# Kernel tuning notes

Hardware: AMD Instinct MI355X
Metric: run time of the kernel (lower is better)

Reference implementation:

```python
import jax, jax.numpy as jnp
import numpy as np

N = 50000
E = 600000
LLM_DIM = 640
HIDDEN = 128
STRUCT_DIM = 16
N_STRUCT_TYPES = 5
N_LAYERS = 2
LN_EPS = 1e-5


def setup_inputs() -> dict:
    key = jax.random.key(0)
    ks = jax.random.split(key, 10)
    llm_feat = jax.random.normal(ks[0], (N, LLM_DIM), dtype=jnp.float32)
    struct_type_ids = jax.random.randint(ks[1], (N,), 0, N_STRUCT_TYPES, dtype=jnp.int64)
    edge_index = jax.random.randint(ks[2], (2, E), 0, N, dtype=jnp.int64)
    proj_out = HIDDEN - STRUCT_DIM  # 112
    proj_W = jax.random.normal(ks[3], (LLM_DIM, proj_out), dtype=jnp.float32) / np.sqrt(LLM_DIM)
    proj_b = jnp.zeros((proj_out,), dtype=jnp.float32)
    struct_emb = jax.random.normal(ks[4], (N_STRUCT_TYPES, STRUCT_DIM), dtype=jnp.float32)
    gcn_W = jax.random.normal(ks[5], (N_LAYERS, HIDDEN, HIDDEN), dtype=jnp.float32) / np.sqrt(HIDDEN)
    gcn_b = jnp.zeros((N_LAYERS, HIDDEN), dtype=jnp.float32)
    ln_g = jnp.ones((HIDDEN,), dtype=jnp.float32)
    ln_b = jnp.zeros((HIDDEN,), dtype=jnp.float32)
    return dict(llm_feat=llm_feat, struct_type_ids=struct_type_ids, edge_index=edge_index,
                proj_W=proj_W, proj_b=proj_b, struct_emb=struct_emb,
                gcn_W=gcn_W, gcn_b=gcn_b, ln_g=ln_g, ln_b=ln_b)


def _gcn_conv(x, src, dst, deg_inv_sqrt, W, b):
    """PyG GCNConv: x' = D^{-1/2}(A+I)D^{-1/2} (x W) + b, D over A+I."""
    xw = x @ W  # [N, H]
    norm = deg_inv_sqrt[src] * deg_inv_sqrt[dst]  # [E]
    msg = xw[src] * norm[:, None]  # [E, H]
    agg = jax.ops.segment_sum(msg, dst, num_segments=N)  # [N, H]
    # self-loop contribution: norm_ii = deg_i^{-1}
    agg = agg + xw * (deg_inv_sqrt * deg_inv_sqrt)[:, None]
    return agg + b


def reference(llm_feat, struct_type_ids, edge_index, proj_W, proj_b,
              struct_emb, gcn_W, gcn_b, ln_g, ln_b):
    x_llm = llm_feat @ proj_W + proj_b  # [N, hidden-struct_dim]
    x_struct = struct_emb[struct_type_ids]  # [N, struct_dim]
    x = jnp.concatenate([x_llm, x_struct], axis=-1)  # [N, hidden]

    src, dst = edge_index[0], edge_index[1]
    # degree with self-loops (A + I)
    deg = 1.0 + jax.ops.segment_sum(jnp.ones((E,), dtype=x.dtype), dst, num_segments=N)
    deg_inv_sqrt = jax.lax.rsqrt(deg)

    for l in range(N_LAYERS):
        x_new = jax.nn.relu(_gcn_conv(x, src, dst, deg_inv_sqrt, gcn_W[l], gcn_b[l]))
        # dropout is identity in eval mode
        x = x + x_new

    mean = jnp.mean(x, axis=-1, keepdims=True)
    var = jnp.mean(jnp.square(x - mean), axis=-1, keepdims=True)
    return (x - mean) * jax.lax.rsqrt(var + LN_EPS) * ln_g + ln_b
```

## Files before the change

kernel.cpp:

```cpp
#include <hip/hip_runtime.h>

#define N_NODES 50000
#define E_EDGES 600000
#define LLM_DIM 640
#define HIDDEN 128
#define POUT 112
#define NB_SCAN 98

typedef __attribute__((ext_vector_type(8))) short bf16x8;
typedef __attribute__((ext_vector_type(4))) float f32x4;

__device__ inline unsigned short f2bf(float f) {
    unsigned u = __float_as_uint(f);
    u += 0x7fff + ((u >> 16) & 1);
    return (unsigned short)(u >> 16);
}
__device__ inline float bflo(unsigned v) { return __uint_as_float(v << 16); }
__device__ inline float bfhi(unsigned v) { return __uint_as_float(v & 0xffff0000u); }

__global__ void deg_count(const int* __restrict__ eidx, int* __restrict__ cnt) {
    int e = blockIdx.x * 256 + threadIdx.x;
    if (e < E_EDGES) atomicAdd(&cnt[eidx[E_EDGES + e]], 1);
}

__global__ void make_dis(const int* __restrict__ cnt, float* __restrict__ dis) {
    int i = blockIdx.x * 256 + threadIdx.x;
    if (i < N_NODES) dis[i] = rsqrtf(1.0f + (float)cnt[i]);
}

__global__ __launch_bounds__(256) void scan_blocksum(const int* __restrict__ cnt, int* __restrict__ bsum) {
    __shared__ int s[256];
    int b = blockIdx.x, t = threadIdx.x;
    int i0 = b * 512 + t, i1 = i0 + 256;
    int v = (i0 < N_NODES ? cnt[i0] : 0) + (i1 < N_NODES ? cnt[i1] : 0);
    s[t] = v;
    __syncthreads();
    for (int st = 128; st; st >>= 1) {
        if (t < st) s[t] += s[t + st];
        __syncthreads();
    }
    if (t == 0) bsum[b] = s[0];
}

__global__ void scan_bsum(const int* __restrict__ bsum, int* __restrict__ bpre) {
    __shared__ int s[128];
    int t = threadIdx.x;
    if (t < NB_SCAN) s[t] = bsum[t];
    __syncthreads();
    if (t == 0) {
        int a = 0;
        for (int i = 0; i < NB_SCAN; i++) { int v = s[i]; s[i] = a; a += v; }
    }
    __syncthreads();
    if (t < NB_SCAN) bpre[t] = s[t];
}

__global__ __launch_bounds__(256) void scan_offs(const int* __restrict__ cnt, const int* __restrict__ bpre,
                                                 int* __restrict__ offs) {
    __shared__ int sA[512], sB[512];
    int b = blockIdx.x, t = threadIdx.x;
    int i0 = b * 512 + t, i1 = i0 + 256;
    int v0 = (i0 < N_NODES ? cnt[i0] : 0);
    int v1 = (i1 < N_NODES ? cnt[i1] : 0);
    sA[t] = v0; sA[t + 256] = v1;
    int* src = sA; int* dst = sB;
    for (int st = 1; st < 512; st <<= 1) {
        __syncthreads();
        dst[t]       = src[t]       + (t       >= st ? src[t - st]       : 0);
        dst[t + 256] = src[t + 256] + (t + 256 >= st ? src[t + 256 - st] : 0);
        int* tmp = src; src = dst; dst = tmp;
    }
    __syncthreads();
    int base = bpre[b];
    if (i0 < N_NODES) offs[i0] = base + src[t] - v0;
    if (i1 < N_NODES) offs[i1] = base + src[t + 256] - v1;
    if (b == 0 && t == 0) offs[N_NODES] = E_EDGES;
}

__global__ void fill_srcs(const int* __restrict__ eidx, const int* __restrict__ offs,
                          int* __restrict__ pos, int* __restrict__ srcs) {
    int e = blockIdx.x * 256 + threadIdx.x;
    if (e >= E_EDGES) return;
    int s = eidx[e];
    int d = eidx[E_EDGES + e];
    int p = atomicAdd(&pos[d], 1);
    srcs[offs[d] + p] = s;
}

__global__ void wt_convert(const float* __restrict__ W, unsigned short* __restrict__ Wt) {
    int idx = blockIdx.x * 256 + threadIdx.x;
    if (idx >= POUT * LLM_DIM) return;
    int n = idx / LLM_DIM;
    int k = idx - n * LLM_DIM;
    Wt[(size_t)n * LLM_DIM + k] = f2bf(W[(size_t)k * POUT + n]);
}

__global__ void w2_convert(const float* __restrict__ W, unsigned short* __restrict__ Wt2) {
    int idx = blockIdx.x * 256 + threadIdx.x;
    if (idx >= 2 * HIDDEN * HIDDEN) return;
    int l = idx >> 14;
    int rem = idx & 16383;
    int n = rem >> 7;
    int k = rem & 127;
    Wt2[idx] = f2bf(W[l * 16384 + k * 128 + n]);
}

__global__ __launch_bounds__(256) void proj_mfma(const float* __restrict__ A,
                                                 const unsigned short* __restrict__ Wt,
                                                 const float* __restrict__ bias,
                                                 const float* __restrict__ emb,
                                                 const int* __restrict__ sid,
                                                 const float* __restrict__ dis,
                                                 float* __restrict__ X,
                                                 unsigned short* __restrict__ Xs) {
    __shared__ short As[64][72];
    __shared__ short Bs[112][72];
    const int tid = threadIdx.x;
    const int wave = tid >> 6, lane = tid & 63;
    const int row0 = blockIdx.x * 64;
    const int l15 = lane & 15, l4 = lane >> 4;

    f32x4 acc[7];
#pragma unroll
    for (int j = 0; j < 7; j++) acc[j] = (f32x4){0.f, 0.f, 0.f, 0.f};

    for (int k0 = 0; k0 < LLM_DIM; k0 += 64) {
#pragma unroll
        for (int i = 0; i < 4; i++) {
            int f = i * 256 + tid;
            int r = f >> 4;
            int q = f & 15;
            int grow = row0 + r;
            float4 v = make_float4(0.f, 0.f, 0.f, 0.f);
            if (grow < N_NODES)
                v = *reinterpret_cast<const float4*>(A + (size_t)grow * LLM_DIM + k0 + q * 4);
            uint2 u;
            u.x = (unsigned)f2bf(v.x) | ((unsigned)f2bf(v.y) << 16);
            u.y = (unsigned)f2bf(v.z) | ((unsigned)f2bf(v.w) << 16);
            *reinterpret_cast<uint2*>(&As[r][q * 4]) = u;
        }
#pragma unroll
        for (int i = 0; i < 7; i++) {
            int f = i * 256 + tid;
            int n = f >> 4;
            int q = f & 15;
            uint2 v = *reinterpret_cast<const uint2*>(Wt + (size_t)n * LLM_DIM + k0 + q * 4);
            *reinterpret_cast<uint2*>(&Bs[n][q * 4]) = v;
        }
        __syncthreads();
#pragma unroll
        for (int ks = 0; ks < 2; ks++) {
            int kk = ks * 32 + l4 * 8;
            bf16x8 a = *reinterpret_cast<bf16x8*>(&As[wave * 16 + l15][kk]);
#pragma unroll
            for (int ct = 0; ct < 7; ct++) {
                bf16x8 b = *reinterpret_cast<bf16x8*>(&Bs[ct * 16 + l15][kk]);
                acc[ct] = __builtin_amdgcn_mfma_f32_16x16x32_bf16(a, b, acc[ct], 0, 0, 0);
            }
        }
        __syncthreads();
    }
#pragma unroll
    for (int r = 0; r < 4; r++) {
        int row = row0 + wave * 16 + l4 * 4 + r;
        if (row >= N_NODES) continue;
        float d = dis[row];
#pragma unroll
        for (int ct = 0; ct < 7; ct++) {
            int col = ct * 16 + l15;
            float v = acc[ct][r] + bias[col];
            X[(size_t)row * HIDDEN + col] = v;
            Xs[(size_t)row * HIDDEN + col] = f2bf(d * v);
        }
        float e = emb[sid[row] * 16 + l15];
        X[(size_t)row * HIDDEN + POUT + l15] = e;
        Xs[(size_t)row * HIDDEN + POUT + l15] = f2bf(d * e);
    }
}

__global__ __launch_bounds__(256) void gather(const unsigned short* __restrict__ Xs,
                                              const int* __restrict__ offs,
                                              const int* __restrict__ srcs,
                                              const float* __restrict__ dis,
                                              unsigned short* __restrict__ Gb) {
    int node = blockIdx.x * 4 + (threadIdx.x >> 6);
    int lane = threadIdx.x & 63;
    if (node >= N_NODES) return;
    int beg = __builtin_amdgcn_readfirstlane(offs[node]);
    int end = __builtin_amdgcn_readfirstlane(offs[node + 1]);
    const unsigned* X32 = reinterpret_cast<const unsigned*>(Xs);
    float ax = 0.f, ay = 0.f;
    int e = beg;
    while (e < end) {
        int n = end - e;
        if (n > 64) n = 64;
        int idx = (lane < n) ? srcs[e + lane] : 0;
        int j = 0;
        for (; j + 4 <= n; j += 4) {
            int s0 = __shfl(idx, j);
            int s1 = __shfl(idx, j + 1);
            int s2 = __shfl(idx, j + 2);
            int s3 = __shfl(idx, j + 3);
            unsigned v0 = X32[(size_t)s0 * 64 + lane];
            unsigned v1 = X32[(size_t)s1 * 64 + lane];
            unsigned v2 = X32[(size_t)s2 * 64 + lane];
            unsigned v3 = X32[(size_t)s3 * 64 + lane];
            ax += (bflo(v0) + bflo(v1)) + (bflo(v2) + bflo(v3));
            ay += (bfhi(v0) + bfhi(v1)) + (bfhi(v2) + bfhi(v3));
        }
        for (; j < n; j++) {
            int s = __shfl(idx, j);
            unsigned v = X32[(size_t)s * 64 + lane];
            ax += bflo(v);
            ay += bfhi(v);
        }
        e += 64;
    }
    float d = dis[node];
    unsigned sv = X32[(size_t)node * 64 + lane];
    ax = d * (ax + bflo(sv));
    ay = d * (ay + bfhi(sv));
    reinterpret_cast<unsigned*>(Gb)[(size_t)node * 64 + lane] =
        (unsigned)f2bf(ax) | ((unsigned)f2bf(ay) << 16);
}

template <int MODE>
__global__ __launch_bounds__(256) void gemm_fin(const unsigned short* __restrict__ Gb,
                                                const unsigned short* __restrict__ Wt2,
                                                const float* __restrict__ bias,
                                                const float* __restrict__ dis,
                                                const float* __restrict__ lng,
                                                const float* __restrict__ lnb,
                                                float* __restrict__ X,
                                                unsigned short* __restrict__ Xs2) {
    __shared__ short As[64][136];
    __shared__ short Bs[128][136];
    const int tid = threadIdx.x;
    const int wave = tid >> 6, lane = tid & 63;
    const int row0 = blockIdx.x * 64;
    const int l15 = lane & 15, l4 = lane >> 4;

#pragma unroll
    for (int i = 0; i < 4; i++) {
        int f = i * 256 + tid;
        int r = f >> 4;
        int q = f & 15;
        int grow = row0 + r;
        uint4 v = make_uint4(0, 0, 0, 0);
        if (grow < N_NODES)
            v = reinterpret_cast<const uint4*>(Gb + (size_t)grow * HIDDEN)[q];
        *reinterpret_cast<uint4*>(&As[r][q * 8]) = v;
    }
#pragma unroll
    for (int i = 0; i < 8; i++) {
        int f = i * 256 + tid;
        int r = f >> 4;
        int q = f & 15;
        uint4 v = reinterpret_cast<const uint4*>(Wt2 + (size_t)r * HIDDEN)[q];
        *reinterpret_cast<uint4*>(&Bs[r][q * 8]) = v;
    }
    __syncthreads();

    f32x4 acc[8];
#pragma unroll
    for (int j = 0; j < 8; j++) acc[j] = (f32x4){0.f, 0.f, 0.f, 0.f};
#pragma unroll
    for (int ks = 0; ks < 4; ks++) {
        int kk = ks * 32 + l4 * 8;
        bf16x8 a = *reinterpret_cast<bf16x8*>(&As[wave * 16 + l15][kk]);
#pragma unroll
        for (int ct = 0; ct < 8; ct++) {
            bf16x8 b = *reinterpret_cast<bf16x8*>(&Bs[ct * 16 + l15][kk]);
            acc[ct] = __builtin_amdgcn_mfma_f32_16x16x32_bf16(a, b, acc[ct], 0, 0, 0);
        }
    }

    float bcol[8];
#pragma unroll
    for (int ct = 0; ct < 8; ct++) bcol[ct] = bias[ct * 16 + l15];

    float vv[8][4];
#pragma unroll
    for (int r = 0; r < 4; r++) {
        int row = row0 + wave * 16 + l4 * 4 + r;
        bool ok = row < N_NODES;
#pragma unroll
        for (int ct = 0; ct < 8; ct++) {
            float xo = ok ? X[(size_t)row * HIDDEN + ct * 16 + l15] : 0.f;
            vv[ct][r] = xo + fmaxf(acc[ct][r] + bcol[ct], 0.f);
        }
    }

    if (MODE == 0) {
#pragma unroll
        for (int r = 0; r < 4; r++) {
            int row = row0 + wave * 16 + l4 * 4 + r;
            if (row >= N_NODES) continue;
            float d = dis[row];
#pragma unroll
            for (int ct = 0; ct < 8; ct++) {
                int col = ct * 16 + l15;
                X[(size_t)row * HIDDEN + col] = vv[ct][r];
                Xs2[(size_t)row * HIDDEN + col] = f2bf(d * vv[ct][r]);
            }
        }
    } else {
        float s[4], q2[4];
#pragma unroll
        for (int r = 0; r < 4; r++) {
            s[r] = 0.f; q2[r] = 0.f;
#pragma unroll
            for (int ct = 0; ct < 8; ct++) {
                s[r] += vv[ct][r];
                q2[r] += vv[ct][r] * vv[ct][r];
            }
        }
#pragma unroll
        for (int off = 1; off < 16; off <<= 1) {
#pragma unroll
            for (int r = 0; r < 4; r++) {
                s[r] += __shfl_xor(s[r], off);
                q2[r] += __shfl_xor(q2[r], off);
            }
        }
        float gcol[8], bcol2[8];
#pragma unroll
        for (int ct = 0; ct < 8; ct++) {
            gcol[ct] = lng[ct * 16 + l15];
            bcol2[ct] = lnb[ct * 16 + l15];
        }
#pragma unroll
        for (int r = 0; r < 4; r++) {
            int row = row0 + wave * 16 + l4 * 4 + r;
            if (row >= N_NODES) continue;
            float mean = s[r] * (1.f / 128.f);
            float var = q2[r] * (1.f / 128.f) - mean * mean;
            float inv = rsqrtf(var + 1e-5f);
#pragma unroll
            for (int ct = 0; ct < 8; ct++) {
                int col = ct * 16 + l15;
                X[(size_t)row * HIDDEN + col] = (vv[ct][r] - mean) * inv * gcol[ct] + bcol2[ct];
            }
        }
    }
}

extern "C" void kernel_launch(void* const* d_in, const int* in_sizes, int n_in,
                              void* d_out, int out_size, void* d_ws, size_t ws_size,
                              hipStream_t stream) {
    const float* llm   = (const float*)d_in[0];
    const int*   sid   = (const int*)d_in[1];
    const int*   eidx  = (const int*)d_in[2];
    const float* projW = (const float*)d_in[3];
    const float* projb = (const float*)d_in[4];
    const float* emb   = (const float*)d_in[5];
    const float* gcnW  = (const float*)d_in[6];
    const float* gcnb  = (const float*)d_in[7];
    const float* lng   = (const float*)d_in[8];
    const float* lnb   = (const float*)d_in[9];

    float* X = (float*)d_out;
    unsigned short* Xs = (unsigned short*)d_ws;
    unsigned short* Gb = Xs + (size_t)N_NODES * HIDDEN;
    unsigned short* Wt = Gb;
    unsigned short* Wt2 = Gb + (size_t)N_NODES * HIDDEN;
    float* dis = (float*)(Wt2 + 2 * HIDDEN * HIDDEN);
    int* cnt  = (int*)(dis + N_NODES);
    int* offs = cnt + N_NODES;
    int* bsum = offs + N_NODES + 1;
    int* bpre = bsum + 128;
    int* srcs = bpre + 128;

    hipMemsetAsync(cnt, 0, N_NODES * sizeof(int), stream);
    deg_count<<<(E_EDGES + 255) / 256, 256, 0, stream>>>(eidx, cnt);
    make_dis<<<(N_NODES + 255) / 256, 256, 0, stream>>>(cnt, dis);
    scan_blocksum<<<NB_SCAN, 256, 0, stream>>>(cnt, bsum);
    scan_bsum<<<1, 128, 0, stream>>>(bsum, bpre);
    scan_offs<<<NB_SCAN, 256, 0, stream>>>(cnt, bpre, offs);
    hipMemsetAsync(cnt, 0, N_NODES * sizeof(int), stream);
    fill_srcs<<<(E_EDGES + 255) / 256, 256, 0, stream>>>(eidx, offs, cnt, srcs);

    wt_convert<<<(POUT * LLM_DIM + 255) / 256, 256, 0, stream>>>(projW, Wt);
    w2_convert<<<(2 * HIDDEN * HIDDEN + 255) / 256, 256, 0, stream>>>(gcnW, Wt2);

    proj_mfma<<<(N_NODES + 63) / 64, 256, 0, stream>>>(llm, Wt, projb, emb, sid, dis, X, Xs);

    gather<<<(N_NODES + 3) / 4, 256, 0, stream>>>(Xs, offs, srcs, dis, Gb);
    gemm_fin<0><<<(N_NODES + 63) / 64, 256, 0, stream>>>(Gb, Wt2, gcnb, dis, lng, lnb, X, Xs);
    gather<<<(N_NODES + 3) / 4, 256, 0, stream>>>(Xs, offs, srcs, dis, Gb);
    gemm_fin<1><<<(N_NODES + 63) / 64, 256, 0, stream>>>(Gb, Wt2 + HIDDEN * HIDDEN, gcnb + HIDDEN, dis, lng, lnb, X, Xs);
}
```

Baseline: 389.5 us.

## Merge weight conversions, fold memsets, unroll gather deeper, prefetch residual in GEMM

```diff
diff --git a/kernel.cpp b/kernel.cpp
--- a/kernel.cpp
+++ b/kernel.cpp
@@ -87,22 +87,23 @@
     srcs[offs[d] + p] = s;
 }
 
-__global__ void wt_convert(const float* __restrict__ W, unsigned short* __restrict__ Wt) {
+__global__ void conv_weights(const float* __restrict__ Wp, const float* __restrict__ Wg,
+                             unsigned short* __restrict__ Wt, unsigned short* __restrict__ Wt2) {
     int idx = blockIdx.x * 256 + threadIdx.x;
-    if (idx >= POUT * LLM_DIM) return;
-    int n = idx / LLM_DIM;
-    int k = idx - n * LLM_DIM;
-    Wt[(size_t)n * LLM_DIM + k] = f2bf(W[(size_t)k * POUT + n]);
-}
-
-__global__ void w2_convert(const float* __restrict__ W, unsigned short* __restrict__ Wt2) {
-    int idx = blockIdx.x * 256 + threadIdx.x;
-    if (idx >= 2 * HIDDEN * HIDDEN) return;
-    int l = idx >> 14;
-    int rem = idx & 16383;
-    int n = rem >> 7;
-    int k = rem & 127;
-    Wt2[idx] = f2bf(W[l * 16384 + k * 128 + n]);
+    if (idx < POUT * LLM_DIM) {
+        int n = idx / LLM_DIM;
+        int k = idx - n * LLM_DIM;
+        Wt[(size_t)n * LLM_DIM + k] = f2bf(Wp[(size_t)k * POUT + n]);
+    } else {
+        int i2 = idx - POUT * LLM_DIM;
+        if (i2 < 2 * HIDDEN * HIDDEN) {
+            int l = i2 >> 14;
+            int rem = i2 & 16383;
+            int n = rem >> 7;
+            int k = rem & 127;
+            Wt2[i2] = f2bf(Wg[l * 16384 + k * 128 + n]);
+        }
+    }
 }
 
 __global__ __launch_bounds__(256) void proj_mfma(const float* __restrict__ A,
@@ -189,6 +190,8 @@
     int beg = __builtin_amdgcn_readfirstlane(offs[node]);
     int end = __builtin_amdgcn_readfirstlane(offs[node + 1]);
     const unsigned* X32 = reinterpret_cast<const unsigned*>(Xs);
+    float d = dis[node];
+    unsigned sv = X32[(size_t)node * 64 + lane];
     float ax = 0.f, ay = 0.f;
     int e = beg;
     while (e < end) {
@@ -196,7 +199,29 @@
         if (n > 64) n = 64;
         int idx = (lane < n) ? srcs[e + lane] : 0;
         int j = 0;
-        for (; j + 4 <= n; j += 4) {
+        for (; j + 8 <= n; j += 8) {
+            int s0 = __shfl(idx, j);
+            int s1 = __shfl(idx, j + 1);
+            int s2 = __shfl(idx, j + 2);
+            int s3 = __shfl(idx, j + 3);
+            int s4 = __shfl(idx, j + 4);
+            int s5 = __shfl(idx, j + 5);
+            int s6 = __shfl(idx, j + 6);
+            int s7 = __shfl(idx, j + 7);
+            unsigned v0 = X32[(size_t)s0 * 64 + lane];
+            unsigned v1 = X32[(size_t)s1 * 64 + lane];
+            unsigned v2 = X32[(size_t)s2 * 64 + lane];
+            unsigned v3 = X32[(size_t)s3 * 64 + lane];
+            unsigned v4 = X32[(size_t)s4 * 64 + lane];
+            unsigned v5 = X32[(size_t)s5 * 64 + lane];
+            unsigned v6 = X32[(size_t)s6 * 64 + lane];
+            unsigned v7 = X32[(size_t)s7 * 64 + lane];
+            ax += ((bflo(v0) + bflo(v1)) + (bflo(v2) + bflo(v3)))
+                + ((bflo(v4) + bflo(v5)) + (bflo(v6) + bflo(v7)));
+            ay += ((bfhi(v0) + bfhi(v1)) + (bfhi(v2) + bfhi(v3)))
+                + ((bfhi(v4) + bfhi(v5)) + (bfhi(v6) + bfhi(v7)));
+        }
+        if (j + 4 <= n) {
             int s0 = __shfl(idx, j);
             int s1 = __shfl(idx, j + 1);
             int s2 = __shfl(idx, j + 2);
@@ -207,17 +232,21 @@
             unsigned v3 = X32[(size_t)s3 * 64 + lane];
             ax += (bflo(v0) + bflo(v1)) + (bflo(v2) + bflo(v3));
             ay += (bfhi(v0) + bfhi(v1)) + (bfhi(v2) + bfhi(v3));
-        }
-        for (; j < n; j++) {
-            int s = __shfl(idx, j);
-            unsigned v = X32[(size_t)s * 64 + lane];
-            ax += bflo(v);
-            ay += bfhi(v);
+            j += 4;
+        }
+        int rem = n - j;
+        if (rem > 0) {
+            int s0 = __shfl(idx, j);
+            int s1 = __shfl(idx, j + (rem > 1 ? 1 : 0));
+            int s2 = __shfl(idx, j + (rem > 2 ? 2 : 0));
+            unsigned v0 = X32[(size_t)s0 * 64 + lane];
+            unsigned v1 = X32[(size_t)s1 * 64 + lane];
+            unsigned v2 = X32[(size_t)s2 * 64 + lane];
+            ax += bflo(v0) + (rem > 1 ? bflo(v1) : 0.f) + (rem > 2 ? bflo(v2) : 0.f);
+            ay += bfhi(v0) + (rem > 1 ? bfhi(v1) : 0.f) + (rem > 2 ? bfhi(v2) : 0.f);
         }
         e += 64;
     }
-    float d = dis[node];
-    unsigned sv = X32[(size_t)node * 64 + lane];
     ax = d * (ax + bflo(sv));
     ay = d * (ay + bfhi(sv));
     reinterpret_cast<unsigned*>(Gb)[(size_t)node * 64 + lane] =
@@ -259,6 +288,17 @@
         uint4 v = reinterpret_cast<const uint4*>(Wt2 + (size_t)r * HIDDEN)[q];
         *reinterpret_cast<uint4*>(&Bs[r][q * 8]) = v;
     }
+
+    float xo[8][4];
+#pragma unroll
+    for (int r = 0; r < 4; r++) {
+        int row = row0 + wave * 16 + l4 * 4 + r;
+        int rc = row < N_NODES ? row : 0;
+#pragma unroll
+        for (int ct = 0; ct < 8; ct++)
+            xo[ct][r] = X[(size_t)rc * HIDDEN + ct * 16 + l15];
+    }
+
     __syncthreads();
 
     f32x4 acc[8];
@@ -286,8 +326,8 @@
         bool ok = row < N_NODES;
 #pragma unroll
         for (int ct = 0; ct < 8; ct++) {
-            float xo = ok ? X[(size_t)row * HIDDEN + ct * 16 + l15] : 0.f;
-            vv[ct][r] = xo + fmaxf(acc[ct][r] + bcol[ct], 0.f);
+            float xv = ok ? xo[ct][r] : 0.f;
+            vv[ct][r] = xv + fmaxf(acc[ct][r] + bcol[ct], 0.f);
         }
     }
 
@@ -366,22 +406,21 @@
     unsigned short* Wt2 = Gb + (size_t)N_NODES * HIDDEN;
     float* dis = (float*)(Wt2 + 2 * HIDDEN * HIDDEN);
     int* cnt  = (int*)(dis + N_NODES);
-    int* offs = cnt + N_NODES;
+    int* pos  = cnt + N_NODES;
+    int* offs = pos + N_NODES;
     int* bsum = offs + N_NODES + 1;
     int* bpre = bsum + 128;
     int* srcs = bpre + 128;
 
-    hipMemsetAsync(cnt, 0, N_NODES * sizeof(int), stream);
+    hipMemsetAsync(cnt, 0, 2 * N_NODES * sizeof(int), stream);
     deg_count<<<(E_EDGES + 255) / 256, 256, 0, stream>>>(eidx, cnt);
     make_dis<<<(N_NODES + 255) / 256, 256, 0, stream>>>(cnt, dis);
     scan_blocksum<<<NB_SCAN, 256, 0, stream>>>(cnt, bsum);
     scan_bsum<<<1, 128, 0, stream>>>(bsum, bpre);
     scan_offs<<<NB_SCAN, 256, 0, stream>>>(cnt, bpre, offs);
-    hipMemsetAsync(cnt, 0, N_NODES * sizeof(int), stream);
-    fill_srcs<<<(E_EDGES + 255) / 256, 256, 0, stream>>>(eidx, offs, cnt, srcs);
-
-    wt_convert<<<(POUT * LLM_DIM + 255) / 256, 256, 0, stream>>>(projW, Wt);
-    w2_convert<<<(2 * HIDDEN * HIDDEN + 255) / 256, 256, 0, stream>>>(gcnW, Wt2);
+    fill_srcs<<<(E_EDGES + 255) / 256, 256, 0, stream>>>(eidx, offs, pos, srcs);
+
+    conv_weights<<<(POUT * LLM_DIM + 2 * HIDDEN * HIDDEN + 255) / 256, 256, 0, stream>>>(projW, gcnW, Wt, Wt2);
 
     proj_mfma<<<(N_NODES + 63) / 64, 256, 0, stream>>>(llm, Wt, projb, emb, sid, dis, X, Xs);
 
```

New measurement: 375.1 us. 1.04x faster.
